# Optimization experiments

Measured on AMD Instinct MI355X. Metric: run time of the kernel, lower is better.

Reference implementation:

```python
import jax, jax.numpy as jnp
import numpy as np

BN_EPS = 1e-5


def setup_inputs() -> dict:
    key = jax.random.key(0)
    ks = jax.random.split(key, 8)
    B, C, H, W_ = 64, 512, 28, 28
    return {
        "x": jax.random.normal(ks[0], (B, C, H, W_), dtype=jnp.float32),
        "rsign_bias": 0.1 * jax.random.normal(ks[1], (C,), dtype=jnp.float32),
        "W": jax.random.normal(ks[2], (C, C), dtype=jnp.float32) * 0.05,  # 1x1 conv weight [out,in]
        "bn_gamma": jnp.ones((C,), dtype=jnp.float32),
        "bn_beta": jnp.zeros((C,), dtype=jnp.float32),
        "bn_mean": 0.1 * jax.random.normal(ks[3], (C,), dtype=jnp.float32),
        "bn_var": jax.random.uniform(ks[4], (C,), dtype=jnp.float32, minval=0.5, maxval=1.5),
        "pr_slope": jax.random.uniform(ks[5], (C,), dtype=jnp.float32, minval=0.1, maxval=0.35),
        "pr_shift": 0.1 * jax.random.normal(ks[6], (C,), dtype=jnp.float32),
        "pr_bias": 0.1 * jax.random.normal(ks[7], (C,), dtype=jnp.float32),
    }


def reference(x, rsign_bias, W, bn_gamma, bn_beta, bn_mean, bn_var,
              pr_slope, pr_shift, pr_bias):
    # x: [B, C, H, W] (NCHW). All params are per-channel [C] except W: [C_out, C_in].
    c = lambda v: v[None, :, None, None]  # broadcast per-channel over NCHW

    # RSign: learnable per-channel shift then binarize (forward = sign)
    a = jnp.sign(x + c(rsign_bias))

    # scaled_sign 1x1 conv: per-output-channel scale = mean(|W|), binarized weight
    scale = jnp.mean(jnp.abs(W), axis=1)          # [C_out]
    Wb = jnp.sign(W) * scale[:, None]             # [C_out, C_in]
    y = jnp.einsum('bchw,oc->bohw', a, Wb)        # 1x1 conv == channel GEMM

    # BatchNorm2d (inference form with running stats)
    bn = c(bn_gamma) * (y - c(bn_mean)) * jax.lax.rsqrt(c(bn_var) + BN_EPS) + c(bn_beta)

    # residual shortcut
    s = bn + x

    # RPReLU: prelu(x - shift) + bias, per-channel learnable slope/shift/bias
    t = s - c(pr_shift)
    out = jnp.where(t > 0, t, c(pr_slope) * t) + c(pr_bias)
    return out
```

## Files before the change

kernel.cpp:

```cpp
#include <hip/hip_runtime.h>
#include <cstdint>

#define C_    512
#define HW_   784
#define B_    64
#define BN_EPS 1e-5f


__global__ __launch_bounds__(64) void precompute_kernel(
    const float* __restrict__ W,
    const float* __restrict__ bn_gamma, const float* __restrict__ bn_beta,
    const float* __restrict__ bn_mean,  const float* __restrict__ bn_var,
    const float* __restrict__ pr_slope, const float* __restrict__ pr_shift,
    const float* __restrict__ pr_bias,
    uint32_t* __restrict__ wbits, float4* __restrict__ params)
{
    const int o    = blockIdx.x;
    const int lane = threadIdx.x;
    const float4* wrow4 = (const float4*)(W + (size_t)o * C_);
    const float4 u = wrow4[2 * lane];
    const float4 v = wrow4[2 * lane + 1];

    float s = fabsf(u.x) + fabsf(u.y) + fabsf(u.z) + fabsf(u.w)
            + fabsf(v.x) + fabsf(v.y) + fabsf(v.z) + fabsf(v.w);
    for (int off = 32; off > 0; off >>= 1) s += __shfl_down(s, off, 64);

    uint32_t m8 = (u.x < 0.f ? 1u : 0u)  | (u.y < 0.f ? 2u : 0u)
                | (u.z < 0.f ? 4u : 0u)  | (u.w < 0.f ? 8u : 0u)
                | (v.x < 0.f ? 16u : 0u) | (v.y < 0.f ? 32u : 0u)
                | (v.z < 0.f ? 64u : 0u) | (v.w < 0.f ? 128u : 0u);

    const uint32_t g0 = __shfl(m8, 4 * lane + 0, 64);
    const uint32_t g1 = __shfl(m8, 4 * lane + 1, 64);
    const uint32_t g2 = __shfl(m8, 4 * lane + 2, 64);
    const uint32_t g3 = __shfl(m8, 4 * lane + 3, 64);
    if (lane < 16)
        wbits[o * 16 + lane] = g0 | (g1 << 8) | (g2 << 16) | (g3 << 24);

    if (lane == 0) {
        float scale = s * (1.0f / (float)C_);
        float r  = rsqrtf(bn_var[o] + BN_EPS);
        float A  = bn_gamma[o] * scale * r;
        float A2 = -2.0f * A;
        float C2 = (float)C_ * A + bn_beta[o] - bn_gamma[o] * bn_mean[o] * r
                 - pr_shift[o];
        params[o] = make_float4(A2, C2, pr_slope[o], pr_bias[o]);
    }
}

__global__ __launch_bounds__(1024, 4) void fused_kernel(
    const float* __restrict__ x, const float* __restrict__ rsign_bias,
    const uint32_t* __restrict__ wbits, const float4* __restrict__ params,
    float* __restrict__ out)
{
    __shared__ uint32_t abits[64 * 17];

    const int i  = threadIdx.x;
    const int jj = __builtin_amdgcn_readfirstlane(threadIdx.y);

    const uint32_t pair = (uint32_t)blockIdx.x * 64u + (uint32_t)i;
    const uint32_t b    = pair / 784u;
    const uint32_t hw   = pair - b * 784u;
    const size_t   base = (size_t)b * (C_ * HW_) + hw;
    const float*   xg   = x + base;

    const int c0 = jj * 32;

    float xv[32];
    #pragma unroll
    for (int t = 0; t < 32; ++t)
        xv[t] = xg[(size_t)(c0 + t) * HW_];

    uint32_t m = 0;
    #pragma unroll
    for (int t = 0; t < 32; ++t) {
        if (xv[t] + rsign_bias[c0 + t] < 0.f) m |= (1u << t);
    }
    abits[i * 17 + jj] = m;
    __syncthreads();

    #pragma unroll
    for (int t = 0; t < 32; ++t) asm volatile("" : "+v"(xv[t]));

    uint32_t a[16];
    #pragma unroll
    for (int w = 0; w < 16; ++w) a[w] = abits[i * 17 + w];

    float* og = out + base;

    #pragma unroll
    for (int oo = 0; oo < 32; ++oo) {
        const int o = c0 + oo;
        const uint32_t* wr = wbits + o * 16;
        int P = 0;
        #pragma unroll
        for (int w = 0; w < 16; ++w) P += __popc(a[w] ^ wr[w]);

        const float4 p = params[o];
        const float t = fmaf(p.x, (float)P, p.y + xv[oo]);
        const float r = fmaf(p.z, fminf(t, 0.f), fmaxf(t, 0.f) + p.w);
        og[(size_t)o * HW_] = r;
    }
}

extern "C" void kernel_launch(void* const* d_in, const int* in_sizes, int n_in,
                              void* d_out, int out_size, void* d_ws, size_t ws_size,
                              hipStream_t stream) {
    const float* x          = (const float*)d_in[0];
    const float* rsign_bias = (const float*)d_in[1];
    const float* W          = (const float*)d_in[2];
    const float* bn_gamma   = (const float*)d_in[3];
    const float* bn_beta    = (const float*)d_in[4];
    const float* bn_mean    = (const float*)d_in[5];
    const float* bn_var     = (const float*)d_in[6];
    const float* pr_slope   = (const float*)d_in[7];
    const float* pr_shift   = (const float*)d_in[8];
    const float* pr_bias    = (const float*)d_in[9];
    float* out = (float*)d_out;

    uint32_t* wbits  = (uint32_t*)d_ws;
    float4*   params = (float4*)((char*)d_ws + 32768);

    precompute_kernel<<<dim3(C_), dim3(64), 0, stream>>>(
        W, bn_gamma, bn_beta, bn_mean, bn_var, pr_slope, pr_shift, pr_bias,
        wbits, params);

    fused_kernel<<<dim3(784), dim3(64, 16), 0, stream>>>(
        x, rsign_bias, wbits, params, out);
}
```

Before: 238.3 us.

## Split fused kernel into separate binarize and popcount-GEMM kernels via workspace

Splits the single 1024-thread fused kernel into a binarize kernel that writes packed sign bits to a global workspace and a separate 128-thread GEMM kernel that reads those bits, recomputes popcounts and reloads x for the residual. The aim is to drop the block-wide __syncthreads and large register footprint so more small blocks can be resident. The cost is an extra kernel launch, a ~3.2 MB bit-plane round trip through global memory, and reading x twice. The fallback fused kernel also now reloads x instead of holding it in registers.

```diff
diff --git a/kernel.cpp b/kernel.cpp
--- a/kernel.cpp
+++ b/kernel.cpp
@@ -1,10 +1,14 @@
 #include <hip/hip_runtime.h>
 #include <cstdint>
 
-#define C_    512
-#define HW_   784
-#define B_    64
+#define C_     512
+#define HW_    784
+#define B_     64
+#define NPAIR  50176
 #define BN_EPS 1e-5f
+
+#define ABITS_OFF 49152
+#define WS_NEEDED (ABITS_OFF + (size_t)NPAIR * 16 * 4)
 
 
 __global__ __launch_bounds__(64) void precompute_kernel(
@@ -48,7 +52,95 @@
     }
 }
 
-__global__ __launch_bounds__(1024, 4) void fused_kernel(
+__global__ __launch_bounds__(128, 8) void binarize_kernel(
+    const float* __restrict__ x, const float* __restrict__ rsign_bias,
+    uint32_t* __restrict__ abits_g)
+{
+    const int lane = threadIdx.x & 63;
+    const int wv   = threadIdx.x >> 6;
+    const uint32_t blk  = blockIdx.x;
+    const uint32_t tile = blk >> 2;
+    const uint32_t wc   = (blk & 3) * 2 + wv;
+
+    const uint32_t pair = tile * 64u + (uint32_t)lane;
+    const uint32_t b    = pair / 784u;
+    const uint32_t hw   = pair - b * 784u;
+    const float*   xg   = x + (size_t)b * (C_ * HW_) + hw;
+
+    const int c0 = (int)wc * 64;
+
+    uint32_t m0 = 0, m1 = 0;
+    #pragma unroll
+    for (int h = 0; h < 4; ++h) {
+        float v[16];
+        #pragma unroll
+        for (int t = 0; t < 16; ++t)
+            v[t] = xg[(size_t)(c0 + h * 16 + t) * HW_];
+        #pragma unroll
+        for (int t = 0; t < 16; ++t) {
+            const int c = h * 16 + t;
+            if (v[t] + rsign_bias[c0 + c] < 0.f) {
+                if (c < 32) m0 |= (1u << c);
+                else        m1 |= (1u << (c - 32));
+            }
+        }
+    }
+    abits_g[(size_t)(2 * wc)     * NPAIR + pair] = m0;
+    abits_g[(size_t)(2 * wc + 1) * NPAIR + pair] = m1;
+}
+
+__global__ __launch_bounds__(128, 8) void gemm_kernel(
+    const float* __restrict__ x, const uint32_t* __restrict__ abits_g,
+    const uint32_t* __restrict__ wbits, const float4* __restrict__ params,
+    float* __restrict__ out)
+{
+    const int lane = threadIdx.x & 63;
+    const int wv   = threadIdx.x >> 6;
+    const uint32_t blk  = blockIdx.x;
+    const uint32_t tile = blk >> 2;
+    const uint32_t oc   = (blk & 3) * 2 + wv;
+
+    const uint32_t pair = tile * 64u + (uint32_t)lane;
+    const uint32_t b    = pair / 784u;
+    const uint32_t hw   = pair - b * 784u;
+    const size_t   base = (size_t)b * (C_ * HW_) + hw;
+    const float*   xg   = x + base;
+    float*         og   = out + base;
+
+    uint32_t a[16];
+    #pragma unroll
+    for (int w = 0; w < 16; ++w)
+        a[w] = abits_g[(size_t)w * NPAIR + pair];
+
+    const int o0 = (int)oc * 64;
+
+    #pragma unroll
+    for (int g = 0; g < 8; ++g) {
+        float xv[8];
+        int   P[8];
+        #pragma unroll
+        for (int u = 0; u < 8; ++u)
+            xv[u] = xg[(size_t)(o0 + g * 8 + u) * HW_];
+        #pragma unroll
+        for (int u = 0; u < 8; ++u) {
+            const uint32_t* wr = wbits + (o0 + g * 8 + u) * 16;
+            int p = 0;
+            #pragma unroll
+            for (int w = 0; w < 16; ++w) p += __popc(a[w] ^ wr[w]);
+            P[u] = p;
+        }
+        #pragma unroll
+        for (int u = 0; u < 8; ++u) {
+            const int o = o0 + g * 8 + u;
+            const float4 pp = params[o];
+            const float t = fmaf(pp.x, (float)P[u], pp.y + xv[u]);
+            const float r = fmaf(pp.z, fminf(t, 0.f), fmaxf(t, 0.f) + pp.w);
+            og[(size_t)o * HW_] = r;
+        }
+    }
+}
+
+__global__ __launch_bounds__(1024, 8) void fused_kernel(
     const float* __restrict__ x, const float* __restrict__ rsign_bias,
     const uint32_t* __restrict__ wbits, const float4* __restrict__ params,
     float* __restrict__ out)
@@ -66,21 +158,18 @@
 
     const int c0 = jj * 32;
 
-    float xv[32];
-    #pragma unroll
-    for (int t = 0; t < 32; ++t)
-        xv[t] = xg[(size_t)(c0 + t) * HW_];
-
-    uint32_t m = 0;
-    #pragma unroll
-    for (int t = 0; t < 32; ++t) {
-        if (xv[t] + rsign_bias[c0 + t] < 0.f) m |= (1u << t);
-    }
-    abits[i * 17 + jj] = m;
+    {
+        float v[32];
+        #pragma unroll
+        for (int t = 0; t < 32; ++t)
+            v[t] = xg[(size_t)(c0 + t) * HW_];
+        uint32_t m = 0;
+        #pragma unroll
+        for (int t = 0; t < 32; ++t)
+            if (v[t] + rsign_bias[c0 + t] < 0.f) m |= (1u << t);
+        abits[i * 17 + jj] = m;
+    }
     __syncthreads();
-
-    #pragma unroll
-    for (int t = 0; t < 32; ++t) asm volatile("" : "+v"(xv[t]));
 
     uint32_t a[16];
     #pragma unroll
@@ -97,7 +186,7 @@
         for (int w = 0; w < 16; ++w) P += __popc(a[w] ^ wr[w]);
 
         const float4 p = params[o];
-        const float t = fmaf(p.x, (float)P, p.y + xv[oo]);
+        const float t = fmaf(p.x, (float)P, p.y + xg[(size_t)o * HW_]);
         const float r = fmaf(p.z, fminf(t, 0.f), fmaxf(t, 0.f) + p.w);
         og[(size_t)o * HW_] = r;
     }
@@ -118,13 +207,21 @@
     const float* pr_bias    = (const float*)d_in[9];
     float* out = (float*)d_out;
 
-    uint32_t* wbits  = (uint32_t*)d_ws;
-    float4*   params = (float4*)((char*)d_ws + 32768);
+    uint32_t* wbits   = (uint32_t*)d_ws;
+    float4*   params  = (float4*)((char*)d_ws + 32768);
+    uint32_t* abits_g = (uint32_t*)((char*)d_ws + ABITS_OFF);
 
     precompute_kernel<<<dim3(C_), dim3(64), 0, stream>>>(
         W, bn_gamma, bn_beta, bn_mean, bn_var, pr_slope, pr_shift, pr_bias,
         wbits, params);
 
-    fused_kernel<<<dim3(784), dim3(64, 16), 0, stream>>>(
-        x, rsign_bias, wbits, params, out);
-}
+    if (ws_size >= WS_NEEDED) {
+        binarize_kernel<<<dim3(3136), dim3(128), 0, stream>>>(
+            x, rsign_bias, abits_g);
+        gemm_kernel<<<dim3(3136), dim3(128), 0, stream>>>(
+            x, abits_g, wbits, params, out);
+    } else {
+        fused_kernel<<<dim3(784), dim3(64, 16), 0, stream>>>(
+            x, rsign_bias, wbits, params, out);
+    }
+}
```

Result: slower. 282.3 us (+18.5%).

## Stage weight bits and params in LDS, reload x instead of holding registers

Applied to the files above, without the earlier changes.

Each block now copies the packed binary weights and per-channel parameters into shared memory and reads them from LDS in the popcount loop instead of from global memory. The 32 x values per thread are no longer kept in registers across the barrier; they are reloaded from global (likely L2/cache hits) in the epilogue. This lowers register pressure so the launch bound can request 8 waves per SIMD. The cost is about 40KB of LDS per block, which may cap occupancy, plus a second read of x.

```diff
diff --git a/kernel.cpp b/kernel.cpp
--- a/kernel.cpp
+++ b/kernel.cpp
@@ -1,9 +1,10 @@
 #include <hip/hip_runtime.h>
 #include <cstdint>
 
-#define C_    512
-#define HW_   784
-#define B_    64
+#define C_     512
+#define HW_    784
+#define B_     64
+#define NPAIR  50176
 #define BN_EPS 1e-5f
 
 
@@ -48,15 +49,18 @@
     }
 }
 
-__global__ __launch_bounds__(1024, 4) void fused_kernel(
+__global__ __launch_bounds__(1024, 8) void fused_kernel(
     const float* __restrict__ x, const float* __restrict__ rsign_bias,
     const uint32_t* __restrict__ wbits, const float4* __restrict__ params,
     float* __restrict__ out)
 {
     __shared__ uint32_t abits[64 * 17];
+    __shared__ uint32_t wlds[512 * 16];
+    __shared__ float4   plds[512];
 
-    const int i  = threadIdx.x;
-    const int jj = __builtin_amdgcn_readfirstlane(threadIdx.y);
+    const int i   = threadIdx.x;
+    const int jj  = __builtin_amdgcn_readfirstlane(threadIdx.y);
+    const int tid = jj * 64 + i;
 
     const uint32_t pair = (uint32_t)blockIdx.x * 64u + (uint32_t)i;
     const uint32_t b    = pair / 784u;
@@ -66,21 +70,27 @@
 
     const int c0 = jj * 32;
 
-    float xv[32];
-    #pragma unroll
-    for (int t = 0; t < 32; ++t)
-        xv[t] = xg[(size_t)(c0 + t) * HW_];
+    const uint4* wsrc = (const uint4*)wbits;
+    const uint4  w0 = wsrc[2 * tid];
+    const uint4  w1 = wsrc[2 * tid + 1];
+    const float2 pp2 = ((const float2*)params)[tid];
 
-    uint32_t m = 0;
-    #pragma unroll
-    for (int t = 0; t < 32; ++t) {
-        if (xv[t] + rsign_bias[c0 + t] < 0.f) m |= (1u << t);
+    {
+        float v[32];
+        #pragma unroll
+        for (int t = 0; t < 32; ++t)
+            v[t] = xg[(size_t)(c0 + t) * HW_];
+        uint32_t m = 0;
+        #pragma unroll
+        for (int t = 0; t < 32; ++t)
+            if (v[t] + rsign_bias[c0 + t] < 0.f) m |= (1u << t);
+        abits[i * 17 + jj] = m;
     }
-    abits[i * 17 + jj] = m;
+
+    ((uint4*)wlds)[2 * tid]     = w0;
+    ((uint4*)wlds)[2 * tid + 1] = w1;
+    ((float2*)plds)[tid]        = pp2;
     __syncthreads();
-
-    #pragma unroll
-    for (int t = 0; t < 32; ++t) asm volatile("" : "+v"(xv[t]));
 
     uint32_t a[16];
     #pragma unroll
@@ -91,13 +101,20 @@
     #pragma unroll
     for (int oo = 0; oo < 32; ++oo) {
         const int o = c0 + oo;
-        const uint32_t* wr = wbits + o * 16;
+        const uint4* wr4 = (const uint4*)(wlds + o * 16);
+        const uint4 q0 = wr4[0], q1 = wr4[1], q2 = wr4[2], q3 = wr4[3];
         int P = 0;
-        #pragma unroll
-        for (int w = 0; w < 16; ++w) P += __popc(a[w] ^ wr[w]);
+        P += __popc(a[0]  ^ q0.x); P += __popc(a[1]  ^ q0.y);
+        P += __popc(a[2]  ^ q0.z); P += __popc(a[3]  ^ q0.w);
+        P += __popc(a[4]  ^ q1.x); P += __popc(a[5]  ^ q1.y);
+        P += __popc(a[6]  ^ q1.z); P += __popc(a[7]  ^ q1.w);
+        P += __popc(a[8]  ^ q2.x); P += __popc(a[9]  ^ q2.y);
+        P += __popc(a[10] ^ q2.z); P += __popc(a[11] ^ q2.w);
+        P += __popc(a[12] ^ q3.x); P += __popc(a[13] ^ q3.y);
+        P += __popc(a[14] ^ q3.z); P += __popc(a[15] ^ q3.w);
 
-        const float4 p = params[o];
-        const float t = fmaf(p.x, (float)P, p.y + xv[oo]);
+        const float4 p = plds[o];
+        const float t = fmaf(p.x, (float)P, p.y + xg[(size_t)o * HW_]);
         const float r = fmaf(p.z, fminf(t, 0.f), fmaxf(t, 0.f) + p.w);
         og[(size_t)o * HW_] = r;
     }
```

Measured after the change: 283.6 us. 19.0% more time.
